# Kernel tuning notes

Measured on AMD Instinct MI355X. Metric: run time of the kernel, lower is better.

The kernel has to match this reference:

```python
import jax, jax.numpy as jnp
import numpy as np

N = 100000
E = 800000
D_IN = 512
D_OUT = 512
EPS = 1e-5


def setup_inputs() -> dict:
    key = jax.random.key(0)
    k = jax.random.split(key, 7)
    x = jax.random.normal(k[0], (N, D_IN), dtype=jnp.float32)
    edge_index = jax.random.randint(k[1], (2, E), 0, N, dtype=jnp.int64)
    # PyG SAGEConv params: lin_l (applied to aggregated neighbors, has bias), lin_r (root weight, no bias)
    W_l = jax.random.normal(k[2], (D_OUT, D_IN), dtype=jnp.float32) * 0.02
    b_l = jnp.zeros((D_OUT,), dtype=jnp.float32)
    W_r = jax.random.normal(k[3], (D_OUT, D_IN), dtype=jnp.float32) * 0.02
    # BatchNorm1d affine params (track_running_stats=False -> always batch stats)
    gamma = jnp.ones((D_OUT,), dtype=jnp.float32)
    beta = jnp.zeros((D_OUT,), dtype=jnp.float32)
    return {"x": x, "edge_index": edge_index, "W_l": W_l, "b_l": b_l,
            "W_r": W_r, "gamma": gamma, "beta": beta}


def reference(x, edge_index, W_l, b_l, W_r, gamma, beta):
    n = x.shape[0]
    src, dst = edge_index[0], edge_index[1]
    # mean-aggregate neighbor features: for each dst node, mean of x[src]
    summed = jax.ops.segment_sum(x[src], dst, num_segments=n)          # [N, D_IN]
    cnt = jax.ops.segment_sum(jnp.ones((src.shape[0],), x.dtype), dst, num_segments=n)
    aggr = summed / jnp.maximum(cnt, 1.0)[:, None]                      # zero-degree -> 0
    # SAGEConv: lin_l(aggr) + lin_r(x)
    h = aggr @ W_l.T + b_l + x @ W_r.T                                  # [N, D_OUT]
    # BatchNorm1d with batch statistics (biased variance), then ReLU
    mu = jnp.mean(h, axis=0)
    var = jnp.mean(jnp.square(h - mu), axis=0)
    h_norm = (h - mu) * jax.lax.rsqrt(var + EPS) * gamma + beta
    return jax.nn.relu(h_norm)
```

## Files before the change

### kernel.cpp

```cpp
#include <hip/hip_runtime.h>
#include <stdint.h>

#define D 512
#define K_TOT 1024
#define EPS 1e-5f
#define CHUNK 1024

typedef __bf16 bf16;
typedef bf16 bf16x4 __attribute__((ext_vector_type(4)));
typedef bf16 bf16x8 __attribute__((ext_vector_type(8)));
typedef float f32x4 __attribute__((ext_vector_type(4)));

__global__ void k_prep(const float* __restrict__ x, bf16* __restrict__ xb,
                       int* __restrict__ cnt, int* __restrict__ cur, float* __restrict__ stat,
                       bf16* __restrict__ padX, bf16* __restrict__ padA,
                       int n, int padGroups, size_t total8) {
  int gid = blockIdx.x * blockDim.x + threadIdx.x;
  if (gid < n) { cnt[gid] = 0; cur[gid] = 0; }
  if (gid < 2 * D) stat[gid] = 0.f;
  if (gid < padGroups) {
    bf16x8 z = {};
    *(bf16x8*)&padX[(size_t)gid * 8] = z;
    *(bf16x8*)&padA[(size_t)gid * 8] = z;
  }
  size_t i = (size_t)gid;
  size_t stride = (size_t)gridDim.x * blockDim.x;
  for (; i < total8; i += stride) {
    float4 a = ((const float4*)x)[i * 2];
    float4 b = ((const float4*)x)[i * 2 + 1];
    bf16x8 v = { (bf16)a.x, (bf16)a.y, (bf16)a.z, (bf16)a.w,
                 (bf16)b.x, (bf16)b.y, (bf16)b.z, (bf16)b.w };
    *(bf16x8*)&xb[i * 8] = v;
  }
}

__global__ void k_degree(const int* __restrict__ dst, int* __restrict__ cnt, int E) {
  int i = blockIdx.x * blockDim.x + threadIdx.x;
  int stride = gridDim.x * blockDim.x;
  for (; i < E; i += stride) atomicAdd(&cnt[dst[i]], 1);
}

__global__ void k_blocksum(const int* __restrict__ cnt, int* __restrict__ bsum, int n) {
  __shared__ int red[4];
  int b = blockIdx.x;
  int base = b * CHUNK;
  int s = 0;
  for (int i = threadIdx.x; i < CHUNK; i += 256) {
    int idx = base + i;
    s += (idx < n) ? cnt[idx] : 0;
  }
#pragma unroll
  for (int o = 32; o > 0; o >>= 1) s += __shfl_down(s, o);
  if ((threadIdx.x & 63) == 0) red[threadIdx.x >> 6] = s;
  __syncthreads();
  if (threadIdx.x == 0) bsum[b] = red[0] + red[1] + red[2] + red[3];
}

__global__ void k_scanb(int* __restrict__ bsum, int* __restrict__ bbase, int nb,
                        int* __restrict__ off, int n, int E) {
  if (threadIdx.x == 0) {
    int run = 0;
    for (int i = 0; i < nb; ++i) { bbase[i] = run; run += bsum[i]; }
    off[n] = E;
  }
}

__global__ void k_offsets(const int* __restrict__ cnt, const int* __restrict__ bbase,
                          int* __restrict__ off, int n) {
  __shared__ int tsum[256];
  int b = blockIdx.x;
  int i0 = b * CHUNK + threadIdx.x * 4;
  int vals[4];
  int s = 0;
#pragma unroll
  for (int j = 0; j < 4; ++j) {
    int idx = i0 + j;
    vals[j] = (idx < n) ? cnt[idx] : 0;
    s += vals[j];
  }
  tsum[threadIdx.x] = s;
  __syncthreads();
  for (int d = 1; d < 256; d <<= 1) {
    int v = (threadIdx.x >= d) ? tsum[threadIdx.x - d] : 0;
    __syncthreads();
    tsum[threadIdx.x] += v;
    __syncthreads();
  }
  int excl = tsum[threadIdx.x] - s + bbase[b];
#pragma unroll
  for (int j = 0; j < 4; ++j) {
    int idx = i0 + j;
    if (idx < n) off[idx] = excl;
    excl += vals[j];
  }
}

__global__ void k_fill(const int* __restrict__ src, const int* __restrict__ dst,
                       const int* __restrict__ off, int* __restrict__ cur,
                       int* __restrict__ csr, int E) {
  int i = blockIdx.x * blockDim.x + threadIdx.x;
  int stride = gridDim.x * blockDim.x;
  for (; i < E; i += stride) {
    int d = dst[i];
    int pos = off[d] + atomicAdd(&cur[d], 1);
    csr[pos] = src[i];
  }
}

__device__ __forceinline__ void acc8(float* c, uint4 u) {
  c[0] += __uint_as_float(u.x << 16);
  c[1] += __uint_as_float(u.x & 0xffff0000u);
  c[2] += __uint_as_float(u.y << 16);
  c[3] += __uint_as_float(u.y & 0xffff0000u);
  c[4] += __uint_as_float(u.z << 16);
  c[5] += __uint_as_float(u.z & 0xffff0000u);
  c[6] += __uint_as_float(u.w << 16);
  c[7] += __uint_as_float(u.w & 0xffff0000u);
}

__global__ __launch_bounds__(256) void k_gather(const bf16* __restrict__ xb,
                                                const int* __restrict__ off,
                                                const int* __restrict__ csr,
                                                bf16* __restrict__ aggr, int n) {
  int node = blockIdx.x * 4 + (threadIdx.x >> 6);
  if (node >= n) return;
  int lane = threadIdx.x & 63;
  int s0 = off[node], s1 = off[node + 1];
  float c[8] = {0.f, 0.f, 0.f, 0.f, 0.f, 0.f, 0.f, 0.f};
  int j = s0;
  for (; j + 7 < s1; j += 8) {
    int i0 = csr[j], i1 = csr[j + 1], i2 = csr[j + 2], i3 = csr[j + 3];
    int i4 = csr[j + 4], i5 = csr[j + 5], i6 = csr[j + 6], i7 = csr[j + 7];
    uint4 u0 = *((const uint4*)(xb + (size_t)i0 * D) + lane);
    uint4 u1 = *((const uint4*)(xb + (size_t)i1 * D) + lane);
    uint4 u2 = *((const uint4*)(xb + (size_t)i2 * D) + lane);
    uint4 u3 = *((const uint4*)(xb + (size_t)i3 * D) + lane);
    uint4 u4 = *((const uint4*)(xb + (size_t)i4 * D) + lane);
    uint4 u5 = *((const uint4*)(xb + (size_t)i5 * D) + lane);
    uint4 u6 = *((const uint4*)(xb + (size_t)i6 * D) + lane);
    uint4 u7 = *((const uint4*)(xb + (size_t)i7 * D) + lane);
    acc8(c, u0); acc8(c, u1); acc8(c, u2); acc8(c, u3);
    acc8(c, u4); acc8(c, u5); acc8(c, u6); acc8(c, u7);
  }
  for (; j + 3 < s1; j += 4) {
    int i0 = csr[j], i1 = csr[j + 1], i2 = csr[j + 2], i3 = csr[j + 3];
    uint4 u0 = *((const uint4*)(xb + (size_t)i0 * D) + lane);
    uint4 u1 = *((const uint4*)(xb + (size_t)i1 * D) + lane);
    uint4 u2 = *((const uint4*)(xb + (size_t)i2 * D) + lane);
    uint4 u3 = *((const uint4*)(xb + (size_t)i3 * D) + lane);
    acc8(c, u0); acc8(c, u1); acc8(c, u2); acc8(c, u3);
  }
  for (; j < s1; ++j) {
    int a = csr[j];
    uint4 u = *((const uint4*)(xb + (size_t)a * D) + lane);
    acc8(c, u);
  }
  float rinv = (s1 > s0) ? 1.0f / (float)(s1 - s0) : 0.0f;
  bf16x8 out = { (bf16)(c[0] * rinv), (bf16)(c[1] * rinv), (bf16)(c[2] * rinv), (bf16)(c[3] * rinv),
                 (bf16)(c[4] * rinv), (bf16)(c[5] * rinv), (bf16)(c[6] * rinv), (bf16)(c[7] * rinv) };
  *(bf16x8*)&aggr[(size_t)node * D + lane * 8] = out;
}

__global__ void k_build_W(const float* __restrict__ Wl, const float* __restrict__ Wr,
                          bf16* __restrict__ Wc) {
  int i = blockIdx.x * blockDim.x + threadIdx.x;
  if (i >= D * K_TOT) return;
  int o = i >> 10, k = i & 1023;
  float v = (k < D) ? Wr[o * D + k] : Wl[o * D + (k - D)];
  Wc[i] = (bf16)v;
}

__device__ __forceinline__ void gl_lds16(const bf16* g, bf16* l) {
  __builtin_amdgcn_global_load_lds((const __attribute__((address_space(1))) unsigned int*)g,
                                   (__attribute__((address_space(3))) unsigned int*)l, 16, 0, 0);
}

template <bool HB>
__global__ __launch_bounds__(512, 2) void k_gemm(const bf16* __restrict__ Xb,
                                                 const bf16* __restrict__ Aggr,
                                                 const bf16* __restrict__ Wc,
                                                 const float* __restrict__ bias,
                                                 bf16* __restrict__ Hb,
                                                 float* __restrict__ Cf,
                                                 float* __restrict__ stat, int M) {
  __shared__ __align__(16) bf16 sA0[256 * 64];
  __shared__ __align__(16) bf16 sB0[256 * 64];
  __shared__ __align__(16) bf16 sA1[256 * 64];
  __shared__ __align__(16) bf16 sB1[256 * 64];
  const int tid = threadIdx.x;
  const int lane = tid & 63;
  const int wid = tid >> 6;
  const int wm = wid >> 2;
  const int wn = wid & 3;
  const int fr = lane & 15;
  const int fq = lane >> 4;

  const int bx = blockIdx.x >> 1;
  const int by = blockIdx.x & 1;
  const size_t rowA0 = (size_t)bx * 256;
  const int rowB0 = by * 256;

  const int lrow = tid >> 3;
  const int scol = (((tid & 7) ^ (lrow & 7)) * 8);
  const bf16* pA_x = Xb + (rowA0 + lrow) * D + scol;
  const bf16* pA_g = Aggr + (rowA0 + lrow) * D + scol;
  const bf16* pB = Wc + (size_t)(rowB0 + lrow) * K_TOT + scol;
  bf16* ldsA0 = &sA0[lrow * 64 + (tid & 7) * 8];
  bf16* ldsB0 = &sB0[lrow * 64 + (tid & 7) * 8];
  bf16* ldsA1 = &sA1[lrow * 64 + (tid & 7) * 8];
  bf16* ldsB1 = &sB1[lrow * 64 + (tid & 7) * 8];

  f32x4 acc[8][4] = {};

#define STAGE(t, la, lb) do {                                                   \
    const bf16* As = ((t) < 8) ? pA_x : pA_g;                                   \
    const int ko = ((t) & 7) * 64;                                              \
    _Pragma("unroll")                                                           \
    for (int i = 0; i < 4; ++i) {                                               \
      gl_lds16(As + (size_t)i * 64 * D + ko, (la) + i * 64 * 64);               \
      gl_lds16(pB + (size_t)i * 64 * K_TOT + (t) * 64, (lb) + i * 64 * 64);     \
    }                                                                           \
  } while (0)

#define COMPUTE(sa, sb) do {                                                    \
    _Pragma("unroll")                                                           \
    for (int kk = 0; kk < 2; ++kk) {                                            \
      const int cx = ((kk * 4 + fq) ^ (fr & 7)) * 8;                            \
      bf16x8 aF[8], bF[4];                                                      \
      _Pragma("unroll")                                                         \
      for (int m = 0; m < 8; ++m)                                               \
        aF[m] = *(const bf16x8*)&(sa)[(wm * 128 + m * 16 + fr) * 64 + cx];      \
      _Pragma("unroll")                                                         \
      for (int nn = 0; nn < 4; ++nn)                                            \
        bF[nn] = *(const bf16x8*)&(sb)[(wn * 64 + nn * 16 + fr) * 64 + cx];     \
      _Pragma("unroll")                                                         \
      for (int m = 0; m < 8; ++m)                                               \
        _Pragma("unroll")                                                       \
        for (int nn = 0; nn < 4; ++nn)                                          \
          acc[m][nn] = __builtin_amdgcn_mfma_f32_16x16x32_bf16(aF[m], bF[nn], acc[m][nn], 0, 0, 0); \
    }                                                                           \
  } while (0)

  STAGE(0, ldsA0, ldsB0);
  __syncthreads();
#pragma unroll 1
  for (int t = 0; t < 16; t += 2) {
    STAGE(t + 1, ldsA1, ldsB1);
    COMPUTE(sA0, sB0);
    __syncthreads();
    if (t + 2 < 16) STAGE(t + 2, ldsA0, ldsB0);
    COMPUTE(sA1, sB1);
    __syncthreads();
  }
#undef STAGE
#undef COMPUTE

  const int rowb = (int)rowA0 + wm * 128;
  const int colb = rowB0 + wn * 64;
  float s[4] = {0.f, 0.f, 0.f, 0.f}, q[4] = {0.f, 0.f, 0.f, 0.f};
#pragma unroll
  for (int nn = 0; nn < 4; ++nn) {
    int col = colb + nn * 16 + fr;
    float bv = bias[col];
#pragma unroll
    for (int m = 0; m < 8; ++m) {
      int row0 = rowb + m * 16 + fq * 4;
#pragma unroll
      for (int r = 0; r < 4; ++r) {
        int row = row0 + r;
        if (row < M) {
          float v = acc[m][nn][r] + bv;
          if (HB) Hb[(size_t)row * D + col] = (bf16)v;
          else    Cf[(size_t)row * D + col] = v;
          s[nn] += v;
          q[nn] += v * v;
        }
      }
    }
  }
#pragma unroll
  for (int nn = 0; nn < 4; ++nn) {
    float sv = s[nn], qv = q[nn];
    sv += __shfl_down(sv, 32); sv += __shfl_down(sv, 16);
    qv += __shfl_down(qv, 32); qv += __shfl_down(qv, 16);
    if (lane < 16) {
      int col = colb + nn * 16 + fr;
      atomicAdd(&stat[col], sv);
      atomicAdd(&stat[D + col], qv);
    }
  }
}

template <bool HB>
__global__ void k_apply(const bf16* __restrict__ hb, const float* __restrict__ hf,
                        const float* __restrict__ stat, const float* __restrict__ gamma,
                        const float* __restrict__ beta, float* __restrict__ out,
                        int n, float invn) {
  size_t i = (size_t)blockIdx.x * blockDim.x + threadIdx.x;
  size_t stride = (size_t)gridDim.x * blockDim.x;
  size_t total = (size_t)n * (D / 4);
  for (; i < total; i += stride) {
    int c4 = ((int)i & 127) * 4;
    float4 v;
    if (HB) {
      bf16x4 hv = *(const bf16x4*)&hb[i * 4];
      v.x = (float)hv[0]; v.y = (float)hv[1]; v.z = (float)hv[2]; v.w = (float)hv[3];
    } else {
      v = ((const float4*)hf)[i];
    }
    float4 st = *(const float4*)&stat[c4];
    float4 sq = *(const float4*)&stat[D + c4];
    float4 gm = *(const float4*)&gamma[c4];
    float4 bt = *(const float4*)&beta[c4];
    float4 o;
    {
      float mu = st.x * invn, var = sq.x * invn - mu * mu;
      float sc = gm.x * rsqrtf(var + EPS);
      o.x = fmaxf(v.x * sc + (bt.x - mu * sc), 0.f);
    }
    {
      float mu = st.y * invn, var = sq.y * invn - mu * mu;
      float sc = gm.y * rsqrtf(var + EPS);
      o.y = fmaxf(v.y * sc + (bt.y - mu * sc), 0.f);
    }
    {
      float mu = st.z * invn, var = sq.z * invn - mu * mu;
      float sc = gm.z * rsqrtf(var + EPS);
      o.z = fmaxf(v.z * sc + (bt.z - mu * sc), 0.f);
    }
    {
      float mu = st.w * invn, var = sq.w * invn - mu * mu;
      float sc = gm.w * rsqrtf(var + EPS);
      o.w = fmaxf(v.w * sc + (bt.w - mu * sc), 0.f);
    }
    ((float4*)out)[i] = o;
  }
}

extern "C" void kernel_launch(void* const* d_in, const int* in_sizes, int n_in,
                              void* d_out, int out_size, void* d_ws, size_t ws_size,
                              hipStream_t stream) {
  const float* x = (const float*)d_in[0];
  const int* ei = (const int*)d_in[1];
  const float* Wl = (const float*)d_in[2];
  const float* bl = (const float*)d_in[3];
  const float* Wr = (const float*)d_in[4];
  const float* gamma = (const float*)d_in[5];
  const float* beta = (const float*)d_in[6];
  float* out = (float*)d_out;

  const int E = in_sizes[1] / 2;
  const int n = in_sizes[0] / D;
  const int Mpad = ((n + 255) / 256) * 256;
  const int nb = (n + CHUNK - 1) / CHUNK;

  char* ws = (char*)d_ws;
  size_t off_b = 0;
  bf16* Xb   = (bf16*)(ws + off_b); off_b += (size_t)Mpad * D * sizeof(bf16);
  bf16* Aggr = (bf16*)(ws + off_b); off_b += (size_t)Mpad * D * sizeof(bf16);
  bf16* Wc   = (bf16*)(ws + off_b); off_b += (size_t)D * K_TOT * sizeof(bf16);
  int* cnt   = (int*)(ws + off_b);  off_b += (size_t)n * sizeof(int);
  int* offs  = (int*)(ws + off_b);  off_b += (size_t)(n + 1) * sizeof(int);
  int* cur   = (int*)(ws + off_b);  off_b += (size_t)n * sizeof(int);
  int* csr   = (int*)(ws + off_b);  off_b += (size_t)E * sizeof(int);
  int* bsum  = (int*)(ws + off_b);  off_b += 512 * sizeof(int);
  int* bbase = (int*)(ws + off_b);  off_b += 512 * sizeof(int);
  float* stat = (float*)(ws + off_b); off_b += 2 * D * sizeof(float);
  bf16* Hb   = (bf16*)(ws + off_b);
  const size_t need_hb = off_b + (size_t)Mpad * D * sizeof(bf16);
  const bool use_hb = (ws_size >= need_hb);

  const int* srcIdx = ei;
  const int* dstIdx = ei + E;
  const int padGroups = (Mpad - n) * D / 8;
  const float invn = 1.0f / (float)n;

  k_prep<<<2048, 256, 0, stream>>>(x, Xb, cnt, cur, stat,
                                   Xb + (size_t)n * D, Aggr + (size_t)n * D,
                                   n, padGroups, (size_t)n * D / 8);
  k_degree<<<1024, 256, 0, stream>>>(dstIdx, cnt, E);
  k_blocksum<<<nb, 256, 0, stream>>>(cnt, bsum, n);
  k_scanb<<<1, 64, 0, stream>>>(bsum, bbase, nb, offs, n, E);
  k_offsets<<<nb, 256, 0, stream>>>(cnt, bbase, offs, n);
  k_fill<<<1024, 256, 0, stream>>>(srcIdx, dstIdx, offs, cur, csr, E);
  k_build_W<<<(D * K_TOT + 255) / 256, 256, 0, stream>>>(Wl, Wr, Wc);
  k_gather<<<(n + 3) / 4, 256, 0, stream>>>(Xb, offs, csr, Aggr, n);
  if (use_hb) {
    k_gemm<true><<<(Mpad / 256) * 2, 512, 0, stream>>>(Xb, Aggr, Wc, bl, Hb, out, stat, n);
    k_apply<true><<<2048, 256, 0, stream>>>(Hb, out, stat, gamma, beta, out, n, invn);
  } else {
    k_gemm<false><<<(Mpad / 256) * 2, 512, 0, stream>>>(Xb, Aggr, Wc, bl, Hb, out, stat, n);
    k_apply<false><<<2048, 256, 0, stream>>>(Hb, out, stat, gamma, beta, out, n, invn);
  }
}
```

Before: 573.0 us.

## Fold GEMM tail tiles into a second pass and stage bf16 output through LDS

The GEMM grid is cut to a multiple of 128 row-blocks. The leftover tail tiles now run as a second pass inside the first blocks, so there is no partial final wave. The bf16 epilogue also writes accumulators into LDS first and then issues coalesced 16-byte row stores to Hb, replacing scattered 2-byte stores. This aims to cut wave-quantization idle time and uncoalesced output writes, at the cost of an extra barrier and some blocks doing twice the work.

```diff
diff --git a/kernel.cpp b/kernel.cpp
--- a/kernel.cpp
+++ b/kernel.cpp
@@ -182,7 +182,8 @@
                                                  const float* __restrict__ bias,
                                                  bf16* __restrict__ Hb,
                                                  float* __restrict__ Cf,
-                                                 float* __restrict__ stat, int M) {
+                                                 float* __restrict__ stat,
+                                                 int nTailTiles, int tailMblkBase, int M) {
   __shared__ __align__(16) bf16 sA0[256 * 64];
   __shared__ __align__(16) bf16 sB0[256 * 64];
   __shared__ __align__(16) bf16 sA1[256 * 64];
@@ -195,22 +196,30 @@
   const int fr = lane & 15;
   const int fq = lane >> 4;
 
-  const int bx = blockIdx.x >> 1;
   const int by = blockIdx.x & 1;
-  const size_t rowA0 = (size_t)bx * 256;
   const int rowB0 = by * 256;
 
   const int lrow = tid >> 3;
   const int scol = (((tid & 7) ^ (lrow & 7)) * 8);
-  const bf16* pA_x = Xb + (rowA0 + lrow) * D + scol;
-  const bf16* pA_g = Aggr + (rowA0 + lrow) * D + scol;
   const bf16* pB = Wc + (size_t)(rowB0 + lrow) * K_TOT + scol;
   bf16* ldsA0 = &sA0[lrow * 64 + (tid & 7) * 8];
   bf16* ldsB0 = &sB0[lrow * 64 + (tid & 7) * 8];
   bf16* ldsA1 = &sA1[lrow * 64 + (tid & 7) * 8];
   bf16* ldsB1 = &sB1[lrow * 64 + (tid & 7) * 8];
 
-  f32x4 acc[8][4] = {};
+  bf16* regbase = (wid < 2) ? sA0 : (wid < 4) ? sB0 : (wid < 6) ? sA1 : sB1;
+  bf16* reg = regbase + (wid & 1) * 8192;
+
+  const int npass = ((int)blockIdx.x < nTailTiles) ? 2 : 1;
+
+#pragma unroll 1
+  for (int pass = 0; pass < npass; ++pass) {
+    const int mblk = pass ? (tailMblkBase + ((int)blockIdx.x >> 1)) : ((int)blockIdx.x >> 1);
+    const size_t rowA0 = (size_t)mblk * 256;
+    const bf16* pA_x = Xb + (rowA0 + lrow) * D + scol;
+    const bf16* pA_g = Aggr + (rowA0 + lrow) * D + scol;
+
+    f32x4 acc[8][4] = {};
 
 #define STAGE(t, la, lb) do {                                                   \
     const bf16* As = ((t) < 8) ? pA_x : pA_g;                                   \
@@ -241,53 +250,65 @@
     }                                                                           \
   } while (0)
 
-  STAGE(0, ldsA0, ldsB0);
-  __syncthreads();
+    STAGE(0, ldsA0, ldsB0);
+    __syncthreads();
 #pragma unroll 1
-  for (int t = 0; t < 16; t += 2) {
-    STAGE(t + 1, ldsA1, ldsB1);
-    COMPUTE(sA0, sB0);
-    __syncthreads();
-    if (t + 2 < 16) STAGE(t + 2, ldsA0, ldsB0);
-    COMPUTE(sA1, sB1);
-    __syncthreads();
-  }
+    for (int t = 0; t < 16; t += 2) {
+      STAGE(t + 1, ldsA1, ldsB1);
+      COMPUTE(sA0, sB0);
+      __syncthreads();
+      if (t + 2 < 16) STAGE(t + 2, ldsA0, ldsB0);
+      COMPUTE(sA1, sB1);
+      __syncthreads();
+    }
 #undef STAGE
 #undef COMPUTE
 
-  const int rowb = (int)rowA0 + wm * 128;
-  const int colb = rowB0 + wn * 64;
-  float s[4] = {0.f, 0.f, 0.f, 0.f}, q[4] = {0.f, 0.f, 0.f, 0.f};
-#pragma unroll
-  for (int nn = 0; nn < 4; ++nn) {
-    int col = colb + nn * 16 + fr;
-    float bv = bias[col];
-#pragma unroll
-    for (int m = 0; m < 8; ++m) {
-      int row0 = rowb + m * 16 + fq * 4;
-#pragma unroll
-      for (int r = 0; r < 4; ++r) {
-        int row = row0 + r;
-        if (row < M) {
+    const int rowb = (int)rowA0 + wm * 128;
+    const int colw = rowB0 + wn * 64;
+    float s[4] = {0.f, 0.f, 0.f, 0.f}, q[4] = {0.f, 0.f, 0.f, 0.f};
+#pragma unroll
+    for (int nn = 0; nn < 4; ++nn) {
+      int col = colw + nn * 16 + fr;
+      float bv = bias[col];
+#pragma unroll
+      for (int m = 0; m < 8; ++m) {
+#pragma unroll
+        for (int r = 0; r < 4; ++r) {
+          int lr = m * 16 + fq * 4 + r;
+          int row = rowb + lr;
           float v = acc[m][nn][r] + bv;
-          if (HB) Hb[(size_t)row * D + col] = (bf16)v;
-          else    Cf[(size_t)row * D + col] = v;
-          s[nn] += v;
-          q[nn] += v * v;
+          if (row < M) { s[nn] += v; q[nn] += v * v; }
+          if (HB) {
+            reg[lr * 64 + nn * 16 + fr] = (bf16)v;
+          } else if (row < M) {
+            Cf[(size_t)row * D + col] = v;
+          }
         }
       }
     }
-  }
-#pragma unroll
-  for (int nn = 0; nn < 4; ++nn) {
-    float sv = s[nn], qv = q[nn];
-    sv += __shfl_down(sv, 32); sv += __shfl_down(sv, 16);
-    qv += __shfl_down(qv, 32); qv += __shfl_down(qv, 16);
-    if (lane < 16) {
-      int col = colb + nn * 16 + fr;
-      atomicAdd(&stat[col], sv);
-      atomicAdd(&stat[D + col], qv);
-    }
+    if (HB) {
+      const int qd = lane >> 3, sd = lane & 7;
+#pragma unroll
+      for (int i = 0; i < 16; ++i) {
+        int lr = i * 8 + qd;
+        int row = rowb + lr;
+        uint4 v = *(const uint4*)&reg[lr * 64 + sd * 8];
+        if (row < M) *(uint4*)&Hb[(size_t)row * D + colw + sd * 8] = v;
+      }
+    }
+#pragma unroll
+    for (int nn = 0; nn < 4; ++nn) {
+      float sv = s[nn], qv = q[nn];
+      sv += __shfl_down(sv, 32); sv += __shfl_down(sv, 16);
+      qv += __shfl_down(qv, 32); qv += __shfl_down(qv, 16);
+      if (lane < 16) {
+        int col = colw + nn * 16 + fr;
+        atomicAdd(&stat[col], sv);
+        atomicAdd(&stat[D + col], qv);
+      }
+    }
+    __syncthreads();
   }
 }
 
@@ -375,6 +396,11 @@
   const int padGroups = (Mpad - n) * D / 8;
   const float invn = 1.0f / (float)n;
 
+  const int mb256 = Mpad / 256;
+  int mainMB = (mb256 / 128) * 128;
+  if (mainMB == 0) mainMB = mb256;
+  const int nTailTiles = (mb256 - mainMB) * 2;
+
   k_prep<<<2048, 256, 0, stream>>>(x, Xb, cnt, cur, stat,
                                    Xb + (size_t)n * D, Aggr + (size_t)n * D,
                                    n, padGroups, (size_t)n * D / 8);
@@ -386,10 +412,12 @@
   k_build_W<<<(D * K_TOT + 255) / 256, 256, 0, stream>>>(Wl, Wr, Wc);
   k_gather<<<(n + 3) / 4, 256, 0, stream>>>(Xb, offs, csr, Aggr, n);
   if (use_hb) {
-    k_gemm<true><<<(Mpad / 256) * 2, 512, 0, stream>>>(Xb, Aggr, Wc, bl, Hb, out, stat, n);
+    k_gemm<true><<<mainMB * 2, 512, 0, stream>>>(Xb, Aggr, Wc, bl, Hb, out, stat,
+                                                 nTailTiles, mainMB, n);
     k_apply<true><<<2048, 256, 0, stream>>>(Hb, out, stat, gamma, beta, out, n, invn);
   } else {
-    k_gemm<false><<<(Mpad / 256) * 2, 512, 0, stream>>>(Xb, Aggr, Wc, bl, Hb, out, stat, n);
+    k_gemm<false><<<mainMB * 2, 512, 0, stream>>>(Xb, Aggr, Wc, bl, Hb, out, stat,
+                                                  nTailTiles, mainMB, n);
     k_apply<false><<<2048, 256, 0, stream>>>(Hb, out, stat, gamma, beta, out, n, invn);
   }
 }
```

Measured after the change: 605.8 us. +5.7%, slower.
